# Optimization experiments

Measured on AMD Instinct MI355X. Metric: run time of the kernel, lower is better.

Reference implementation:

```python
import jax, jax.numpy as jnp
import numpy as np

B, S, D_IN, D, H = 2, 2048, 512, 1024, 16
HD = D // H


def _linear_params(key, d_in, d_out):
    kw, kb = jax.random.split(key)
    bound = 1.0 / np.sqrt(d_in)
    W = jax.random.uniform(kw, (d_in, d_out), jnp.float32, -bound, bound)
    b = jax.random.uniform(kb, (d_out,), jnp.float32, -bound, bound)
    return W, b


def setup_inputs() -> dict:
    key = jax.random.key(0)
    keys = jax.random.split(key, 8)
    x = jax.random.normal(keys[0], (B, S, D_IN), jnp.float32)
    We, be = _linear_params(keys[1], D_IN, D)
    Wq, bq = _linear_params(keys[2], D, D)
    Wk, bk = _linear_params(keys[3], D, D)
    Wv, bv = _linear_params(keys[4], D, D)
    W0, b0 = _linear_params(keys[5], D, D)
    W1, b1 = _linear_params(keys[6], D, D)
    W2, b2 = _linear_params(keys[7], D, D)
    return {"x": x, "We": We, "be": be, "Wq": Wq, "bq": bq, "Wk": Wk, "bk": bk,
            "Wv": Wv, "bv": bv, "W0": W0, "b0": b0, "W1": W1, "b1": b1, "W2": W2, "b2": b2}


def reference(x, We, be, Wq, bq, Wk, bk, Wv, bv, W0, b0, W1, b1, W2, b2):
    # embedding
    e = x @ We + be                                   # [B,S,D]
    q = (e @ Wq + bq).reshape(B, S, H, HD)            # [B,S,H,hd]
    k = (e @ Wk + bk).reshape(B, S, H, HD)
    v = (e @ Wv + bv).reshape(B, S, H, HD)
    scale = 1.0 / jnp.sqrt(jnp.float32(HD))
    scores = jnp.einsum('bqhd,bkhd->bhqk', q, k) * scale
    attn = jax.nn.softmax(scores, axis=-1)            # [B,H,S,S]
    ctx = jnp.einsum('bhqk,bkhd->bqhd', attn, v).reshape(B, S, D)
    mha = e + (ctx @ W0 + b0)                         # residual
    ffn = jax.nn.relu(mha @ W1 + b1) @ W2 + b2
    return mha + ffn
```

## Files before the change

kernel.cpp:

```cpp
#include <hip/hip_runtime.h>

typedef unsigned short u16;
typedef __bf16 bf16x8 __attribute__((ext_vector_type(8)));
typedef float f32x4 __attribute__((ext_vector_type(4)));

__device__ __forceinline__ float bf2f(u16 u) {
  return __builtin_bit_cast(float, (unsigned)u << 16);
}
__device__ __forceinline__ u16 f2bf(float f) {
  unsigned u = __builtin_bit_cast(unsigned, f);
  u += 0x7FFFu + ((u >> 16) & 1u);
  return (u16)(u >> 16);
}
__device__ __forceinline__ unsigned pk2(float a, float b) {
  return (unsigned)f2bf(a) | ((unsigned)f2bf(b) << 16);
}
__device__ __forceinline__ unsigned pk2t(float a, float b) {
  return __builtin_amdgcn_perm(__builtin_bit_cast(unsigned, b),
                               __builtin_bit_cast(unsigned, a), 0x07060302u);
}
__device__ __forceinline__ f32x4 mfma16(bf16x8 a, bf16x8 b, f32x4 c) {
  return __builtin_amdgcn_mfma_f32_16x16x32_bf16(a, b, c, 0, 0, 0);
}
__device__ __forceinline__ void async_cp16(const u16* g, u16* l) {
  __builtin_amdgcn_global_load_lds((const __attribute__((address_space(1))) void*)g,
                                   (__attribute__((address_space(3))) void*)l, 16, 0, 0);
}
#define S_BARRIER() asm volatile("s_barrier" ::: "memory")

__global__ __launch_bounds__(256) void cast_f32_bf16(const float* __restrict__ in,
                                                     u16* __restrict__ out, int n) {
  int idx = (blockIdx.x * 256 + threadIdx.x) * 4;
  if (idx < n) {
    float4 f = *(const float4*)&in[idx];
    ushort4 o;
    o.x = f2bf(f.x); o.y = f2bf(f.y); o.z = f2bf(f.z); o.w = f2bf(f.w);
    *(ushort4*)&out[idx] = o;
  }
}

__global__ __launch_bounds__(256) void biascat(const float* __restrict__ bq,
                                               const float* __restrict__ bk,
                                               const float* __restrict__ bv,
                                               float* __restrict__ o) {
  int i = blockIdx.x * 256 + threadIdx.x;
  if (i < 3072)
    o[i] = i < 1024 ? bq[i] : (i < 2048 ? bk[i - 1024] : bv[i - 2048]);
}

#define TSP 72
__global__ __launch_bounds__(256) void transpose_weights(
    const float* __restrict__ We, const float* __restrict__ Wq,
    const float* __restrict__ Wk, const float* __restrict__ Wv,
    const float* __restrict__ W0, const float* __restrict__ W1,
    const float* __restrict__ W2, u16* Wet, u16* qkvWt, u16* W0t, u16* W1t,
    u16* W2t) {
  const int z = blockIdx.z;
  const float* in;
  u16* out;
  int out_rs = 1024;
  if (z == 0) { if (blockIdx.y >= 8) return; in = We; out = Wet; out_rs = 512; }
  else if (z == 1) { in = Wq; out = qkvWt; }
  else if (z == 2) { in = Wk; out = qkvWt + 1048576; }
  else if (z == 3) { in = Wv; out = qkvWt + 2097152; }
  else if (z == 4) { in = W0; out = W0t; }
  else if (z == 5) { in = W1; out = W1t; }
  else { in = W2; out = W2t; }
  __shared__ alignas(16) u16 T[64][TSP];
  const int tid = threadIdx.x;
  const int r0 = blockIdx.y * 64, c0 = blockIdx.x * 64;
#pragma unroll
  for (int it = 0; it < 4; ++it) {
    int vi = it * 256 + tid;
    int i = vi >> 4, j4 = (vi & 15) * 4;
    float4 f = *(const float4*)&in[(size_t)(r0 + i) * 1024 + c0 + j4];
    T[i][j4 + 0] = f2bf(f.x);
    T[i][j4 + 1] = f2bf(f.y);
    T[i][j4 + 2] = f2bf(f.z);
    T[i][j4 + 3] = f2bf(f.w);
  }
  __syncthreads();
#pragma unroll
  for (int it = 0; it < 2; ++it) {
    int vi = it * 256 + tid;
    int i = vi >> 3, j8 = (vi & 7) * 8;
    bf16x8 v;
#pragma unroll
    for (int u = 0; u < 8; ++u) ((u16*)&v)[u] = T[j8 + u][i];
    *(bf16x8*)&out[(size_t)(c0 + i) * out_rs + r0 + j8] = v;
  }
}

template <int TM>
__global__ __launch_bounds__(256, (TM == 128) ? 3 : 5) void gemm_mfma(
    const u16* __restrict__ A, const u16* __restrict__ Bt,
    const float* __restrict__ bias, const u16* __restrict__ res,
    void* __restrict__ Cout, int M, int N, int K, int relu, int f32out) {
  constexpr int MT = TM / 32;
  constexpr int AI = TM / 32;
  __shared__ alignas(16) u16 As[2][TM * 64];
  __shared__ alignas(16) u16 Bs[2][64 * 64];
  const int tid = threadIdx.x;
  const int wave = tid >> 6, lane = tid & 63;
  const int quad = lane >> 4, l16 = lane & 15;
  const int ib = blockIdx.x;
  int by, bx;
  if constexpr (TM == 128) { by = (ib & 7) * 4 + ((ib >> 3) & 3); bx = ib >> 5; }
  else { by = (ib & 7) * 8 + ((ib >> 3) & 7); bx = ib >> 6; }
  const int m0 = by * TM, n0 = bx * 64;
  const int wm = (wave & 1) * (TM / 2), wn = (wave >> 1) * 32;

  f32x4 acc[MT][2];
#pragma unroll
  for (int i = 0; i < MT; ++i)
#pragma unroll
    for (int j = 0; j < 2; ++j) acc[i][j] = (f32x4){0.f, 0.f, 0.f, 0.f};

  const int srow = lane >> 3;
  const int schunk = (lane & 7) ^ (srow & 7);
  const u16* Ag = A + (size_t)(m0 + wave * (TM / 4) + srow) * K + schunk * 8;
  const u16* Bg = Bt + (size_t)(n0 + wave * 16 + srow) * K + schunk * 8;
  u16* AsW0 = &As[0][wave * (TM / 4) * 64];
  u16* BsW0 = &Bs[0][wave * 16 * 64];
  u16* AsW1 = &As[1][wave * (TM / 4) * 64];
  u16* BsW1 = &Bs[1][wave * 16 * 64];

#define GEMM_ISSUE(ab, bb, k)                                     \
  {                                                               \
    _Pragma("unroll") for (int i = 0; i < AI; ++i)                \
        async_cp16(Ag + (k) + (size_t)i * 8 * K, (ab) + i * 512); \
    _Pragma("unroll") for (int i = 0; i < 2; ++i)                 \
        async_cp16(Bg + (k) + (size_t)i * 8 * K, (bb) + i * 512); \
  }

  GEMM_ISSUE(AsW0, BsW0, 0);
  const int T = K >> 6;
  const int swz = (l16 & 7);
  for (int t = 0; t < T; ++t) {
    const int cb = t & 1;
    S_BARRIER();
    const int kn = (t + 1 < T) ? ((t + 1) << 6) : 0;
    if (cb == 0) GEMM_ISSUE(AsW1, BsW1, kn) else GEMM_ISSUE(AsW0, BsW0, kn);
    if constexpr (TM == 128)
      asm volatile("s_waitcnt vmcnt(6)" ::: "memory");
    else
      asm volatile("s_waitcnt vmcnt(4)" ::: "memory");
    S_BARRIER();
#pragma unroll
    for (int kk = 0; kk < 2; ++kk) {
      bf16x8 af[MT], bfr[2];
#pragma unroll
      for (int mt = 0; mt < MT; ++mt)
        af[mt] = *(const bf16x8*)&As[cb][(wm + mt * 16 + l16) * 64 +
                                        ((kk * 4 + quad) ^ swz) * 8];
#pragma unroll
      for (int nt = 0; nt < 2; ++nt)
        bfr[nt] = *(const bf16x8*)&Bs[cb][(wn + nt * 16 + l16) * 64 +
                                          ((kk * 4 + quad) ^ swz) * 8];
#pragma unroll
      for (int mt = 0; mt < MT; ++mt)
#pragma unroll
        for (int nt = 0; nt < 2; ++nt)
          acc[mt][nt] = mfma16(af[mt], bfr[nt], acc[mt][nt]);
    }
  }
  asm volatile("s_waitcnt vmcnt(0)" ::: "memory");

#pragma unroll
  for (int nt = 0; nt < 2; ++nt) {
    int col = n0 + wn + nt * 16 + l16;
    float bv = bias[col];
#pragma unroll
    for (int mt = 0; mt < MT; ++mt) {
#pragma unroll
      for (int r = 0; r < 4; ++r) {
        int row = m0 + wm + mt * 16 + quad * 4 + r;
        float v = acc[mt][nt][r] + bv;
        if (res) v += bf2f(res[(size_t)row * N + col]);
        if (relu) v = fmaxf(v, 0.f);
        if (f32out)
          ((float*)Cout)[(size_t)row * N + col] = v;
        else
          ((u16*)Cout)[(size_t)row * N + col] = f2bf(v);
      }
    }
  }
}

__global__ __launch_bounds__(256, 2) void attn_kernel(
    const u16* __restrict__ QKV, const u16* __restrict__ Vt,
    u16* __restrict__ O) {
  __shared__ alignas(16) u16 Ks[2][64 * 64];
  __shared__ alignas(16) u16 Vs[2][64 * 64];
  __shared__ alignas(16) u16 Ps[4][32 * 72];
  const int tid = threadIdx.x;
  const int wave = tid >> 6, lane = tid & 63;
  const int quad = lane >> 4, l16 = lane & 15;
  const int ib = blockIdx.x;
  const int bh = ib & 31, b = bh >> 4, h = bh & 15;
  const int q0 = (ib >> 5) * 128 + wave * 32;

  bf16x8 qf[2][2];
#pragma unroll
  for (int qt = 0; qt < 2; ++qt) {
    const size_t qoff = (size_t)(b * 2048 + q0 + qt * 16 + l16) * 3072 + h * 64;
#pragma unroll
    for (int kk = 0; kk < 2; ++kk) {
      bf16x8 raw = *(const bf16x8*)&QKV[qoff + kk * 32 + quad * 8];
#pragma unroll
      for (int u = 0; u < 8; ++u)
        ((u16*)&raw)[u] = f2bf(0.125f * bf2f(((u16*)&raw)[u]));
      qf[qt][kk] = raw;
    }
  }
  bf16x8 ones;
#pragma unroll
  for (int u = 0; u < 8; ++u) ((u16*)&ones)[u] = 0x3F80;

  f32x4 o[4][2];
  f32x4 l_acc[2] = {(f32x4){0.f, 0.f, 0.f, 0.f}, (f32x4){0.f, 0.f, 0.f, 0.f}};
#pragma unroll
  for (int mt = 0; mt < 4; ++mt)
#pragma unroll
    for (int qt = 0; qt < 2; ++qt) o[mt][qt] = (f32x4){0.f, 0.f, 0.f, 0.f};

  const int srow = lane >> 3;
  const int schunk = (lane & 7) ^ (srow & 7);
  const u16* Kg = QKV + (size_t)(b * 2048 + wave * 16 + srow) * 3072 + 1024 +
                  h * 64 + schunk * 8;
  const u16* Vg = Vt + (size_t)((b * 16 + h) * 64 + wave * 16 + srow) * 2048 +
                  schunk * 8;
  u16* KsW0 = &Ks[0][(wave * 16) * 64];
  u16* VsW0 = &Vs[0][(wave * 16) * 64];
  u16* KsW1 = &Ks[1][(wave * 16) * 64];
  u16* VsW1 = &Vs[1][(wave * 16) * 64];

#define ATTN_ISSUE(kb, vb, kt)                                \
  {                                                           \
    async_cp16(Kg + (size_t)(kt) * 3072, (kb));               \
    async_cp16(Kg + (size_t)((kt) + 8) * 3072, (kb) + 512);   \
    async_cp16(Vg + (kt), (vb));                              \
    async_cp16(Vg + (kt) + (size_t)8 * 2048, (vb) + 512);     \
  }

  ATTN_ISSUE(KsW0, VsW0, 0);
  const int swz = (l16 & 7);
  u16* PsW = &Ps[wave][0];
  for (int t = 0; t < 32; ++t) {
    const int cb = t & 1;
    S_BARRIER();
    const int ktn = (t + 1 < 32) ? ((t + 1) * 64) : 0;
    if (cb == 0) ATTN_ISSUE(KsW1, VsW1, ktn) else ATTN_ISSUE(KsW0, VsW0, ktn);
    asm volatile("s_waitcnt vmcnt(4)" ::: "memory");
    S_BARRIER();

    f32x4 st[4][2];
#pragma unroll
    for (int km = 0; km < 4; ++km)
#pragma unroll
      for (int qt = 0; qt < 2; ++qt) st[km][qt] = (f32x4){0.f, 0.f, 0.f, 0.f};
#pragma unroll
    for (int kk = 0; kk < 2; ++kk)
#pragma unroll
      for (int km = 0; km < 4; ++km) {
        bf16x8 kf = *(const bf16x8*)&Ks[cb][(km * 16 + l16) * 64 +
                                           ((kk * 4 + quad) ^ swz) * 8];
        st[km][0] = mfma16(kf, qf[0][kk], st[km][0]);
        st[km][1] = mfma16(kf, qf[1][kk], st[km][1]);
      }

#pragma unroll
    for (int qt = 0; qt < 2; ++qt)
#pragma unroll
      for (int km = 0; km < 4; ++km) {
        float e0 = __expf(st[km][qt][0]), e1 = __expf(st[km][qt][1]);
        float e2 = __expf(st[km][qt][2]), e3 = __expf(st[km][qt][3]);
        uint2 pk;
        pk.x = pk2t(e0, e1);
        pk.y = pk2t(e2, e3);
        *(uint2*)&PsW[(qt * 16 + l16) * 72 + km * 16 + quad * 4] = pk;
      }
    asm volatile("s_waitcnt lgkmcnt(0)" ::: "memory");

#pragma unroll
    for (int kk2 = 0; kk2 < 2; ++kk2) {
      bf16x8 pf0 = *(const bf16x8*)&PsW[l16 * 72 + kk2 * 32 + quad * 8];
      bf16x8 pf1 = *(const bf16x8*)&PsW[(16 + l16) * 72 + kk2 * 32 + quad * 8];
      l_acc[0] = mfma16(ones, pf0, l_acc[0]);
      l_acc[1] = mfma16(ones, pf1, l_acc[1]);
#pragma unroll
      for (int mt = 0; mt < 4; ++mt) {
        bf16x8 vf = *(const bf16x8*)&Vs[cb][(mt * 16 + l16) * 64 +
                                           ((kk2 * 4 + quad) ^ swz) * 8];
        o[mt][0] = mfma16(vf, pf0, o[mt][0]);
        o[mt][1] = mfma16(vf, pf1, o[mt][1]);
      }
    }
  }
  asm volatile("s_waitcnt vmcnt(0)" ::: "memory");

#pragma unroll
  for (int qt = 0; qt < 2; ++qt) {
    float inv = 1.f / l_acc[qt][0];
    size_t base = (size_t)(b * 2048 + q0 + qt * 16 + l16) * 1024 + h * 64;
#pragma unroll
    for (int mt = 0; mt < 4; ++mt) {
      uint2 pk;
      pk.x = pk2(o[mt][qt][0] * inv, o[mt][qt][1] * inv);
      pk.y = pk2(o[mt][qt][2] * inv, o[mt][qt][3] * inv);
      *(uint2*)&O[base + mt * 16 + quad * 4] = pk;
    }
  }
}

__global__ __launch_bounds__(256) void transpose_v(const u16* __restrict__ QKV,
                                                   u16* __restrict__ vt) {
  const int bh = blockIdx.y;
  const int b = bh >> 4, h = bh & 15;
  const int s0 = blockIdx.x * 64;
  const u16* in = QKV + (size_t)b * 2048 * 3072 + 2048 + h * 64;
  u16* out = vt + (size_t)bh * 131072;
  __shared__ alignas(16) u16 T[64][TSP];
  const int tid = threadIdx.x;
#pragma unroll
  for (int it = 0; it < 2; ++it) {
    int vi = it * 256 + tid;
    int i = vi >> 3, j8 = (vi & 7) * 8;
    *(bf16x8*)&T[i][j8] = *(const bf16x8*)&in[(size_t)(s0 + i) * 3072 + j8];
  }
  __syncthreads();
#pragma unroll
  for (int it = 0; it < 2; ++it) {
    int vi = it * 256 + tid;
    int i = vi >> 3, j8 = (vi & 7) * 8;
    bf16x8 vv;
#pragma unroll
    for (int u = 0; u < 8; ++u) ((u16*)&vv)[u] = T[j8 + u][i];
    *(bf16x8*)&out[(size_t)i * 2048 + s0 + j8] = vv;
  }
}

extern "C" void kernel_launch(void* const* d_in, const int* in_sizes, int n_in,
                              void* d_out, int out_size, void* d_ws,
                              size_t ws_size, hipStream_t stream) {
  const float* x = (const float*)d_in[0];
  const float* We = (const float*)d_in[1];
  const float* be = (const float*)d_in[2];
  const float* Wq = (const float*)d_in[3];
  const float* bq = (const float*)d_in[4];
  const float* Wk = (const float*)d_in[5];
  const float* bk = (const float*)d_in[6];
  const float* Wv = (const float*)d_in[7];
  const float* bv = (const float*)d_in[8];
  const float* W0 = (const float*)d_in[9];
  const float* b0 = (const float*)d_in[10];
  const float* W1 = (const float*)d_in[11];
  const float* b1 = (const float*)d_in[12];
  const float* W2 = (const float*)d_in[13];
  const float* b2 = (const float*)d_in[14];

  u16* ws = (u16*)d_ws;
  u16* xb = ws;
  u16* Wet = xb + 2097152;
  u16* qkvWt = Wet + 524288;
  u16* ctx = ws;
  u16* W0t = qkvWt + 3145728;
  u16* W1t = W0t + 1048576;
  u16* W2t = W1t + 1048576;
  float* biasqkv = (float*)(W2t + 1048576);
  u16* e = W2t + 1048576 + 6144;
  u16* qkv = e + 4194304;
  u16* vtb = qkv + 12582912;
  u16* mha = qkv;
  u16* h1 = e;

  cast_f32_bf16<<<2048, 256, 0, stream>>>(x, xb, 4096 * 512);
  transpose_weights<<<dim3(16, 16, 7), 256, 0, stream>>>(
      We, Wq, Wk, Wv, W0, W1, W2, Wet, qkvWt, W0t, W1t, W2t);
  biascat<<<12, 256, 0, stream>>>(bq, bk, bv, biasqkv);

  gemm_mfma<64><<<1024, 256, 0, stream>>>(xb, Wet, be, nullptr, e, 4096, 1024,
                                          512, 0, 0);
  gemm_mfma<128><<<1536, 256, 0, stream>>>(e, qkvWt, biasqkv, nullptr, qkv,
                                           4096, 3072, 1024, 0, 0);
  transpose_v<<<dim3(32, 32), 256, 0, stream>>>(qkv, vtb);
  attn_kernel<<<512, 256, 0, stream>>>(qkv, vtb, ctx);
  gemm_mfma<64><<<1024, 256, 0, stream>>>(ctx, W0t, b0, e, mha, 4096, 1024,
                                          1024, 0, 0);
  gemm_mfma<64><<<1024, 256, 0, stream>>>(mha, W1t, b1, nullptr, h1, 4096,
                                          1024, 1024, 1, 0);
  gemm_mfma<64><<<1024, 256, 0, stream>>>(h1, W2t, b2, mha, d_out, 4096, 1024,
                                          1024, 0, 1);
}
```

Baseline: 258.9 us.

## Shrink attention query tile per wave to 16 rows and double block count

Each wave in the attention kernel now handles 16 query rows instead of 32, so the grid doubles to 1024 blocks and launch bounds request 4 blocks per CU. The P scratch buffer is changed to an XOR-swizzled 16x64 layout without padding, and s_setprio is raised around the MFMA sections. The aim is more waves in flight to hide latency and fewer LDS bank conflicts. The cost is that K/V tiles are loaded and staged twice as often per query row, so there is less reuse of LDS data per MFMA.

```diff
diff --git a/kernel.cpp b/kernel.cpp
--- a/kernel.cpp
+++ b/kernel.cpp
@@ -187,42 +187,39 @@
   }
 }
 
-__global__ __launch_bounds__(256, 2) void attn_kernel(
+__global__ __launch_bounds__(256, 4) void attn_kernel(
     const u16* __restrict__ QKV, const u16* __restrict__ Vt,
     u16* __restrict__ O) {
   __shared__ alignas(16) u16 Ks[2][64 * 64];
   __shared__ alignas(16) u16 Vs[2][64 * 64];
-  __shared__ alignas(16) u16 Ps[4][32 * 72];
+  __shared__ alignas(16) u16 Ps[4][16 * 64];
   const int tid = threadIdx.x;
   const int wave = tid >> 6, lane = tid & 63;
   const int quad = lane >> 4, l16 = lane & 15;
   const int ib = blockIdx.x;
   const int bh = ib & 31, b = bh >> 4, h = bh & 15;
-  const int q0 = (ib >> 5) * 128 + wave * 32;
-
-  bf16x8 qf[2][2];
-#pragma unroll
-  for (int qt = 0; qt < 2; ++qt) {
-    const size_t qoff = (size_t)(b * 2048 + q0 + qt * 16 + l16) * 3072 + h * 64;
+  const int q0 = (ib >> 5) * 64 + wave * 16;
+
+  bf16x8 qf[2];
+  {
+    const size_t qoff = (size_t)(b * 2048 + q0 + l16) * 3072 + h * 64;
 #pragma unroll
     for (int kk = 0; kk < 2; ++kk) {
       bf16x8 raw = *(const bf16x8*)&QKV[qoff + kk * 32 + quad * 8];
 #pragma unroll
       for (int u = 0; u < 8; ++u)
         ((u16*)&raw)[u] = f2bf(0.125f * bf2f(((u16*)&raw)[u]));
-      qf[qt][kk] = raw;
+      qf[kk] = raw;
     }
   }
   bf16x8 ones;
 #pragma unroll
   for (int u = 0; u < 8; ++u) ((u16*)&ones)[u] = 0x3F80;
 
-  f32x4 o[4][2];
-  f32x4 l_acc[2] = {(f32x4){0.f, 0.f, 0.f, 0.f}, (f32x4){0.f, 0.f, 0.f, 0.f}};
-#pragma unroll
-  for (int mt = 0; mt < 4; ++mt)
-#pragma unroll
-    for (int qt = 0; qt < 2; ++qt) o[mt][qt] = (f32x4){0.f, 0.f, 0.f, 0.f};
+  f32x4 o[4];
+  f32x4 l_acc = (f32x4){0.f, 0.f, 0.f, 0.f};
+#pragma unroll
+  for (int mt = 0; mt < 4; ++mt) o[mt] = (f32x4){0.f, 0.f, 0.f, 0.f};
 
   const int srow = lane >> 3;
   const int schunk = (lane & 7) ^ (srow & 7);
@@ -254,60 +251,56 @@
     asm volatile("s_waitcnt vmcnt(4)" ::: "memory");
     S_BARRIER();
 
-    f32x4 st[4][2];
-#pragma unroll
-    for (int km = 0; km < 4; ++km)
-#pragma unroll
-      for (int qt = 0; qt < 2; ++qt) st[km][qt] = (f32x4){0.f, 0.f, 0.f, 0.f};
+    f32x4 st[4];
+#pragma unroll
+    for (int km = 0; km < 4; ++km) st[km] = (f32x4){0.f, 0.f, 0.f, 0.f};
+    __builtin_amdgcn_s_setprio(1);
 #pragma unroll
     for (int kk = 0; kk < 2; ++kk)
 #pragma unroll
       for (int km = 0; km < 4; ++km) {
         bf16x8 kf = *(const bf16x8*)&Ks[cb][(km * 16 + l16) * 64 +
                                            ((kk * 4 + quad) ^ swz) * 8];
-        st[km][0] = mfma16(kf, qf[0][kk], st[km][0]);
-        st[km][1] = mfma16(kf, qf[1][kk], st[km][1]);
+        st[km] = mfma16(kf, qf[kk], st[km]);
       }
-
-#pragma unroll
-    for (int qt = 0; qt < 2; ++qt)
-#pragma unroll
-      for (int km = 0; km < 4; ++km) {
-        float e0 = __expf(st[km][qt][0]), e1 = __expf(st[km][qt][1]);
-        float e2 = __expf(st[km][qt][2]), e3 = __expf(st[km][qt][3]);
-        uint2 pk;
-        pk.x = pk2t(e0, e1);
-        pk.y = pk2t(e2, e3);
-        *(uint2*)&PsW[(qt * 16 + l16) * 72 + km * 16 + quad * 4] = pk;
-      }
+    __builtin_amdgcn_s_setprio(0);
+
+#pragma unroll
+    for (int km = 0; km < 4; ++km) {
+      float e0 = __expf(st[km][0]), e1 = __expf(st[km][1]);
+      float e2 = __expf(st[km][2]), e3 = __expf(st[km][3]);
+      uint2 pk;
+      pk.x = pk2t(e0, e1);
+      pk.y = pk2t(e2, e3);
+      *(uint2*)&PsW[l16 * 64 + ((km * 2 + (quad >> 1)) ^ swz) * 8 +
+                    (quad & 1) * 4] = pk;
+    }
     asm volatile("s_waitcnt lgkmcnt(0)" ::: "memory");
 
+    __builtin_amdgcn_s_setprio(1);
 #pragma unroll
     for (int kk2 = 0; kk2 < 2; ++kk2) {
-      bf16x8 pf0 = *(const bf16x8*)&PsW[l16 * 72 + kk2 * 32 + quad * 8];
-      bf16x8 pf1 = *(const bf16x8*)&PsW[(16 + l16) * 72 + kk2 * 32 + quad * 8];
-      l_acc[0] = mfma16(ones, pf0, l_acc[0]);
-      l_acc[1] = mfma16(ones, pf1, l_acc[1]);
+      bf16x8 pf = *(const bf16x8*)&PsW[l16 * 64 + ((kk2 * 4 + quad) ^ swz) * 8];
+      l_acc = mfma16(ones, pf, l_acc);
 #pragma unroll
       for (int mt = 0; mt < 4; ++mt) {
         bf16x8 vf = *(const bf16x8*)&Vs[cb][(mt * 16 + l16) * 64 +
                                            ((kk2 * 4 + quad) ^ swz) * 8];
-        o[mt][0] = mfma16(vf, pf0, o[mt][0]);
-        o[mt][1] = mfma16(vf, pf1, o[mt][1]);
+        o[mt] = mfma16(vf, pf, o[mt]);
       }
     }
+    __builtin_amdgcn_s_setprio(0);
   }
   asm volatile("s_waitcnt vmcnt(0)" ::: "memory");
 
-#pragma unroll
-  for (int qt = 0; qt < 2; ++qt) {
-    float inv = 1.f / l_acc[qt][0];
-    size_t base = (size_t)(b * 2048 + q0 + qt * 16 + l16) * 1024 + h * 64;
+  {
+    float inv = 1.f / l_acc[0];
+    size_t base = (size_t)(b * 2048 + q0 + l16) * 1024 + h * 64;
 #pragma unroll
     for (int mt = 0; mt < 4; ++mt) {
       uint2 pk;
-      pk.x = pk2(o[mt][qt][0] * inv, o[mt][qt][1] * inv);
-      pk.y = pk2(o[mt][qt][2] * inv, o[mt][qt][3] * inv);
+      pk.x = pk2(o[mt][0] * inv, o[mt][1] * inv);
+      pk.y = pk2(o[mt][2] * inv, o[mt][3] * inv);
       *(uint2*)&O[base + mt * 16 + quad * 4] = pk;
     }
   }
@@ -384,7 +377,7 @@
   gemm_mfma<128><<<1536, 256, 0, stream>>>(e, qkvWt, biasqkv, nullptr, qkv,
                                            4096, 3072, 1024, 0, 0);
   transpose_v<<<dim3(32, 32), 256, 0, stream>>>(qkv, vtb);
-  attn_kernel<<<512, 256, 0, stream>>>(qkv, vtb, ctx);
+  attn_kernel<<<1024, 256, 0, stream>>>(qkv, vtb, ctx);
   gemm_mfma<64><<<1024, 256, 0, stream>>>(ctx, W0t, b0, e, mha, 4096, 1024,
                                           1024, 0, 0);
   gemm_mfma<64><<<1024, 256, 0, stream>>>(mha, W1t, b1, nullptr, h1, 4096,
```

Result: no change. 262.8 us (+1.5%).

## Load K/V fragments directly from global into registers, drop LDS staging and barriers

Applied to the files above, without the earlier changes.

The attention kernel no longer stages K and V tiles through shared memory with async copies and block barriers. Each wave now loads its own K and V MFMA fragments straight from global memory into registers, with K double-buffered one tile ahead. It also adds s_setprio around the MFMA sections and XOR-swizzles the P scratch buffer instead of padding it. This removes the barrier synchronisation and LDS traffic, but each of the four waves now fetches the same K/V separately, which multiplies global/L2 reads and raises register pressure.

```diff
diff --git a/kernel.cpp b/kernel.cpp
--- a/kernel.cpp
+++ b/kernel.cpp
@@ -190,9 +190,7 @@
 __global__ __launch_bounds__(256, 2) void attn_kernel(
     const u16* __restrict__ QKV, const u16* __restrict__ Vt,
     u16* __restrict__ O) {
-  __shared__ alignas(16) u16 Ks[2][64 * 64];
-  __shared__ alignas(16) u16 Vs[2][64 * 64];
-  __shared__ alignas(16) u16 Ps[4][32 * 72];
+  __shared__ alignas(16) u16 Ps[4][32 * 64];
   const int tid = threadIdx.x;
   const int wave = tid >> 6, lane = tid & 63;
   const int quad = lane >> 4, l16 = lane & 15;
@@ -224,80 +222,75 @@
 #pragma unroll
     for (int qt = 0; qt < 2; ++qt) o[mt][qt] = (f32x4){0.f, 0.f, 0.f, 0.f};
 
-  const int srow = lane >> 3;
-  const int schunk = (lane & 7) ^ (srow & 7);
-  const u16* Kg = QKV + (size_t)(b * 2048 + wave * 16 + srow) * 3072 + 1024 +
-                  h * 64 + schunk * 8;
-  const u16* Vg = Vt + (size_t)((b * 16 + h) * 64 + wave * 16 + srow) * 2048 +
-                  schunk * 8;
-  u16* KsW0 = &Ks[0][(wave * 16) * 64];
-  u16* VsW0 = &Vs[0][(wave * 16) * 64];
-  u16* KsW1 = &Ks[1][(wave * 16) * 64];
-  u16* VsW1 = &Vs[1][(wave * 16) * 64];
-
-#define ATTN_ISSUE(kb, vb, kt)                                \
-  {                                                           \
-    async_cp16(Kg + (size_t)(kt) * 3072, (kb));               \
-    async_cp16(Kg + (size_t)((kt) + 8) * 3072, (kb) + 512);   \
-    async_cp16(Vg + (kt), (vb));                              \
-    async_cp16(Vg + (kt) + (size_t)8 * 2048, (vb) + 512);     \
-  }
-
-  ATTN_ISSUE(KsW0, VsW0, 0);
-  const int swz = (l16 & 7);
+  const u16* Kp = QKV + (size_t)(b * 2048 + l16) * 3072 + 1024 + h * 64 + quad * 8;
+  const u16* Vp = Vt + (size_t)((b * 16 + h) * 64 + l16) * 2048 + quad * 8;
   u16* PsW = &Ps[wave][0];
-  for (int t = 0; t < 32; ++t) {
-    const int cb = t & 1;
-    S_BARRIER();
-    const int ktn = (t + 1 < 32) ? ((t + 1) * 64) : 0;
-    if (cb == 0) ATTN_ISSUE(KsW1, VsW1, ktn) else ATTN_ISSUE(KsW0, VsW0, ktn);
-    asm volatile("s_waitcnt vmcnt(4)" ::: "memory");
-    S_BARRIER();
-
-    f32x4 st[4][2];
-#pragma unroll
-    for (int km = 0; km < 4; ++km)
-#pragma unroll
-      for (int qt = 0; qt < 2; ++qt) st[km][qt] = (f32x4){0.f, 0.f, 0.f, 0.f};
-#pragma unroll
-    for (int kk = 0; kk < 2; ++kk)
-#pragma unroll
-      for (int km = 0; km < 4; ++km) {
-        bf16x8 kf = *(const bf16x8*)&Ks[cb][(km * 16 + l16) * 64 +
-                                           ((kk * 4 + quad) ^ swz) * 8];
-        st[km][0] = mfma16(kf, qf[0][kk], st[km][0]);
-        st[km][1] = mfma16(kf, qf[1][kk], st[km][1]);
-      }
-
-#pragma unroll
-    for (int qt = 0; qt < 2; ++qt)
-#pragma unroll
-      for (int km = 0; km < 4; ++km) {
-        float e0 = __expf(st[km][qt][0]), e1 = __expf(st[km][qt][1]);
-        float e2 = __expf(st[km][qt][2]), e3 = __expf(st[km][qt][3]);
-        uint2 pk;
-        pk.x = pk2t(e0, e1);
-        pk.y = pk2t(e2, e3);
-        *(uint2*)&PsW[(qt * 16 + l16) * 72 + km * 16 + quad * 4] = pk;
-      }
-    asm volatile("s_waitcnt lgkmcnt(0)" ::: "memory");
-
-#pragma unroll
-    for (int kk2 = 0; kk2 < 2; ++kk2) {
-      bf16x8 pf0 = *(const bf16x8*)&PsW[l16 * 72 + kk2 * 32 + quad * 8];
-      bf16x8 pf1 = *(const bf16x8*)&PsW[(16 + l16) * 72 + kk2 * 32 + quad * 8];
-      l_acc[0] = mfma16(ones, pf0, l_acc[0]);
-      l_acc[1] = mfma16(ones, pf1, l_acc[1]);
-#pragma unroll
-      for (int mt = 0; mt < 4; ++mt) {
-        bf16x8 vf = *(const bf16x8*)&Vs[cb][(mt * 16 + l16) * 64 +
-                                           ((kk2 * 4 + quad) ^ swz) * 8];
-        o[mt][0] = mfma16(vf, pf0, o[mt][0]);
-        o[mt][1] = mfma16(vf, pf1, o[mt][1]);
-      }
-    }
-  }
-  asm volatile("s_waitcnt vmcnt(0)" ::: "memory");
+  const int swz = l16 & 7;
+
+  bf16x8 kA[4][2], kB[4][2], vf[4][2];
+
+#define LOAD_K(dst, tk)                                                       \
+  {                                                                           \
+    _Pragma("unroll") for (int km = 0; km < 4; ++km)                          \
+    _Pragma("unroll") for (int kk = 0; kk < 2; ++kk)                          \
+        dst[km][kk] = *(const bf16x8*)&Kp[(size_t)((tk)*64 + km * 16) * 3072 +\
+                                          kk * 32];                           \
+  }
+
+#define LOAD_V(tv)                                                            \
+  {                                                                           \
+    _Pragma("unroll") for (int mt = 0; mt < 4; ++mt)                          \
+    _Pragma("unroll") for (int kk = 0; kk < 2; ++kk)                          \
+        vf[mt][kk] = *(const bf16x8*)&Vp[(size_t)(mt * 16) * 2048 + (tv)*64 + \
+                                         kk * 32];                            \
+  }
+
+#define ATTN_STEP(KC, KN, tc)                                                 \
+  {                                                                           \
+    LOAD_V(tc);                                                               \
+    LOAD_K(KN, ((tc) + 1 < 32) ? (tc) + 1 : 0);                               \
+    _Pragma("unroll") for (int qt = 0; qt < 2; ++qt) {                        \
+      f32x4 st[4];                                                            \
+      _Pragma("unroll") for (int km = 0; km < 4; ++km)                        \
+          st[km] = (f32x4){0.f, 0.f, 0.f, 0.f};                               \
+      __builtin_amdgcn_s_setprio(1);                                          \
+      _Pragma("unroll") for (int kk = 0; kk < 2; ++kk)                        \
+      _Pragma("unroll") for (int km = 0; km < 4; ++km)                        \
+          st[km] = mfma16(KC[km][kk], qf[qt][kk], st[km]);                    \
+      __builtin_amdgcn_s_setprio(0);                                          \
+      _Pragma("unroll") for (int km = 0; km < 4; ++km) {                      \
+        float e0 = __expf(st[km][0]), e1 = __expf(st[km][1]);                 \
+        float e2 = __expf(st[km][2]), e3 = __expf(st[km][3]);                 \
+        uint2 pk;                                                             \
+        pk.x = pk2t(e0, e1);                                                  \
+        pk.y = pk2t(e2, e3);                                                  \
+        *(uint2*)&PsW[(qt * 16 + l16) * 64 +                                  \
+                      ((km * 2 + (quad >> 1)) ^ swz) * 8 + (quad & 1) * 4] =  \
+            pk;                                                               \
+      }                                                                       \
+    }                                                                         \
+    asm volatile("s_waitcnt lgkmcnt(0)" ::: "memory");      \
+    __builtin_amdgcn_s_setprio(1);                                            \
+    _Pragma("unroll") for (int kk = 0; kk < 2; ++kk) {                        \
+      bf16x8 pf0 =                                                            \
+          *(const bf16x8*)&PsW[l16 * 64 + ((kk * 4 + quad) ^ swz) * 8];       \
+      bf16x8 pf1 = *(const bf16x8*)&PsW[(16 + l16) * 64 +                     \
+                                        ((kk * 4 + quad) ^ swz) * 8];         \
+      l_acc[0] = mfma16(ones, pf0, l_acc[0]);                                 \
+      l_acc[1] = mfma16(ones, pf1, l_acc[1]);                                 \
+      _Pragma("unroll") for (int mt = 0; mt < 4; ++mt) {                      \
+        o[mt][0] = mfma16(vf[mt][kk], pf0, o[mt][0]);                         \
+        o[mt][1] = mfma16(vf[mt][kk], pf1, o[mt][1]);                         \
+      }                                                                       \
+    }                                                                         \
+    __builtin_amdgcn_s_setprio(0);                                            \
+  }
+
+  LOAD_K(kA, 0);
+  for (int t = 0; t < 32; t += 2) {
+    ATTN_STEP(kA, kB, t);
+    ATTN_STEP(kB, kA, t + 1);
+  }
 
 #pragma unroll
   for (int qt = 0; qt < 2; ++qt) {
```

New measurement: 327.9 us. +26.7%, slower.
